# Kernel tuning notes

Hardware: AMD Instinct MI355X
Metric: run time of the kernel (lower is better)

The kernel has to match this reference:

```python
import jax, jax.numpy as jnp
import numpy as np

DIM = 512
NUM_HEADS = 8
HEAD_DIM = DIM // NUM_HEADS
SCALE = HEAD_DIM ** -0.5


def setup_inputs() -> dict:
    key = jax.random.key(0)
    k1, k2, k3, k4 = jax.random.split(key, 4)
    x = jax.random.normal(k1, (2, 4096, DIM), dtype=jnp.float32)
    # Linear weights stored as (in, out) for x @ W; torch Linear(dim, 3*dim, bias=False)
    w_qkv = jax.random.normal(k2, (DIM, 3 * DIM), dtype=jnp.float32) * (DIM ** -0.5)
    w_proj = jax.random.normal(k3, (DIM, DIM), dtype=jnp.float32) * (DIM ** -0.5)
    b_proj = jax.random.normal(k4, (DIM,), dtype=jnp.float32) * 0.02
    return {"x": x, "w_qkv": w_qkv, "w_proj": w_proj, "b_proj": b_proj}


def reference(x, w_qkv, w_proj, b_proj):
    B, N, C = x.shape
    qkv = (x @ w_qkv).reshape(B, N, 3, NUM_HEADS, HEAD_DIM)
    qkv = jnp.transpose(qkv, (2, 0, 3, 1, 4))  # (3, B, H, N, hd)
    q, k, v = qkv[0], qkv[1], qkv[2]
    attn = jnp.einsum("bhnd,bhmd->bhnm", q, k) * SCALE
    attn = jax.nn.softmax(attn, axis=-1)
    out = jnp.einsum("bhnm,bhmd->bhnd", attn, v)
    out = jnp.transpose(out, (0, 2, 1, 3)).reshape(B, N, C)
    return out @ w_proj + b_proj
```

## Files before the change

kernel.cpp:

```cpp
#include <hip/hip_runtime.h>
#include <hip/hip_bf16.h>
#include <stdint.h>
#include <math.h>

#define NC3 1536
#define NC2 1024
#define QSCALE 0.18033688011111907f
#define KSPLIT 2

typedef __attribute__((ext_vector_type(8))) short short8;
typedef __attribute__((ext_vector_type(4))) short short4v;
typedef __attribute__((ext_vector_type(4))) float f32x4;
typedef __attribute__((ext_vector_type(16))) float f32x16;
typedef __attribute__((ext_vector_type(8))) _Float16 f16x8;
typedef __attribute__((ext_vector_type(2))) _Float16 half2v;
typedef __attribute__((ext_vector_type(2))) __fp16 fp16x2;

static __device__ __forceinline__ short f2bf(float f) {
    union { __hip_bfloat16 h; short s; } u;
    u.h = __float2bfloat16(f);
    return u.s;
}
static __device__ __forceinline__ short f2h(float f) {
    union { __fp16 h; short s; } u;
    u.h = (__fp16)f;
    return u.s;
}
static __device__ __forceinline__ unsigned hpack(float a, float b) {
    union { fp16x2 h; unsigned u; } c;
    c.h = __builtin_amdgcn_cvt_pkrtz(a, b);
    return c.u;
}
static __device__ __forceinline__ float dot2acc(unsigned pu, float c) {
    union { unsigned u; half2v h; } a;
    a.u = pu;
#if __has_builtin(__builtin_amdgcn_fdot2)
    half2v one2 = {(_Float16)1.0f, (_Float16)1.0f};
    return __builtin_amdgcn_fdot2(a.h, one2, c, false);
#else
    return c + (float)a.h[0] + (float)a.h[1];
#endif
}

#define GLD_LDS(g, l)                                                          \
    __builtin_amdgcn_global_load_lds(                                          \
        (const __attribute__((address_space(1))) void*)(g),                    \
        (__attribute__((address_space(3))) void*)(l), 16, 0, 0)

__global__ __launch_bounds__(256) void prep(const float* __restrict__ x,
                                            short* __restrict__ xbf,
                                            const float* __restrict__ wqkv,
                                            short* __restrict__ wqkvT,
                                            const float* __restrict__ wproj,
                                            short* __restrict__ wprojT) {
    int tx = threadIdx.x, ty = threadIdx.y;
    int tid = ty * 32 + tx;
    if (blockIdx.z == 0) {
        int bid = blockIdx.y * 48 + blockIdx.x;
        for (int i = bid * 256 + tid; i < 1048576; i += 768 * 256) {
            float4 v = ((const float4*)x)[i];
            short4v o = {f2bf(v.x), f2bf(v.y), f2bf(v.z), f2bf(v.w)};
            ((short4v*)xbf)[i] = o;
        }
        return;
    }
    const float* src;
    short* dst;
    int C;
    bool tof16;
    if (blockIdx.z == 1) { src = wqkv; dst = wqkvT; C = 1536; tof16 = false; }
    else                 { if (blockIdx.x >= 16) return; src = wproj; dst = wprojT; C = 512; tof16 = true; }
    __shared__ short t[32][33];
    int c0 = blockIdx.x * 32, r0 = blockIdx.y * 32;
#pragma unroll
    for (int i = 0; i < 4; i++) {
        float v = src[(size_t)(r0 + ty + i * 8) * C + c0 + tx];
        t[ty + i * 8][tx] = tof16 ? f2h(v) : f2bf(v);
    }
    __syncthreads();
#pragma unroll
    for (int i = 0; i < 4; i++)
        dst[(size_t)(c0 + ty + i * 8) * 512 + r0 + tx] = t[tx][ty + i * 8];
}

__global__ __launch_bounds__(256) void gemm_qkv(const short* __restrict__ A,
                                                const short* __restrict__ Bt,
                                                short* __restrict__ Out,
                                                short* __restrict__ VT) {
    __shared__ __attribute__((aligned(16))) short smem[2][128 * 64];
    short* a_sm = &smem[0][0];
    short* b_sm = &smem[1][0];
    const int tid = threadIdx.x;
    const int lane = tid & 63;
    const int wave = tid >> 6;
    const int wr = wave >> 1, wc = wave & 1;
    const int quad = lane >> 4;
    const int l15 = lane & 15;
    const int orig = blockIdx.y * 64 + blockIdx.x;
    const int xcd = orig & 7;
    const int lid = orig >> 3;
    const int m0 = (xcd * 8 + (lid & 7)) * 128;
    const int n0 = (lid >> 3) * 128;
    const int srow = lane >> 3;
    const int schunk = (lane & 7) ^ srow;

    f32x4 zero4 = {0.f, 0.f, 0.f, 0.f};
    f32x4 acc[4][4];
#pragma unroll
    for (int i = 0; i < 4; i++)
#pragma unroll
        for (int j = 0; j < 4; j++) acc[i][j] = zero4;

    for (int k0 = 0; k0 < 512; k0 += 64) {
        __syncthreads();
#pragma unroll
        for (int i = 0; i < 4; i++) {
            int r0 = wave * 32 + i * 8;
            GLD_LDS(A + (size_t)(m0 + r0 + srow) * 512 + k0 + schunk * 8, a_sm + r0 * 64);
            GLD_LDS(Bt + (size_t)(n0 + r0 + srow) * 512 + k0 + schunk * 8, b_sm + r0 * 64);
        }
        __syncthreads();
#pragma unroll
        for (int kk = 0; kk < 2; kk++) {
            short8 af[4], bfr[4];
#pragma unroll
            for (int mi = 0; mi < 4; mi++) {
                int row = wr * 64 + mi * 16 + l15;
                af[mi] = *(const short8*)(a_sm + row * 64 + (((kk * 4 + quad) ^ (row & 7))) * 8);
            }
#pragma unroll
            for (int ni = 0; ni < 4; ni++) {
                int row = wc * 64 + ni * 16 + l15;
                bfr[ni] = *(const short8*)(b_sm + row * 64 + (((kk * 4 + quad) ^ (row & 7))) * 8);
            }
#pragma unroll
            for (int mi = 0; mi < 4; mi++)
#pragma unroll
                for (int ni = 0; ni < 4; ni++)
                    acc[mi][ni] = __builtin_amdgcn_mfma_f32_16x16x32_bf16(
                        af[mi], bfr[ni], acc[mi][ni], 0, 0, 0);
        }
    }

    if (n0 < 1024) {
#pragma unroll
        for (int mi = 0; mi < 4; mi++) {
#pragma unroll
            for (int ni = 0; ni < 4; ni++) {
                int gm0 = m0 + wr * 64 + mi * 16 + quad * 4;
                int gn = n0 + wc * 64 + ni * 16 + l15;
                f32x4 v = acc[mi][ni];
#pragma unroll
                for (int r = 0; r < 4; r++) {
                    float val = v[r];
                    float o = (gn < 512) ? val * QSCALE : val;
                    Out[(size_t)(gm0 + r) * NC2 + gn] = f2bf(o);
                }
            }
        }
    }

    if (n0 >= 1024) {
        __syncthreads();
        short* lt = &smem[0][0];
        const int sq = ((quad & 1) << 1) | (quad >> 1);
#pragma unroll
        for (int mi = 0; mi < 4; mi++) {
#pragma unroll
            for (int ni = 0; ni < 4; ni++) {
                int cl = wc * 64 + ni * 16 + l15;
                int tg = wr * 16 + mi * 4 + sq;
                int tg2 = tg ^ ((cl & 7) << 1);
                f32x4 v = acc[mi][ni];
                uint2 pk;
                pk.x = hpack(v[0], v[1]);
                pk.y = hpack(v[2], v[3]);
                *(uint2*)(lt + cl * 128 + tg2 * 4) = pk;
            }
        }
        __syncthreads();
        int cl = tid >> 1, half = tid & 1;
        int cv = n0 - 1024 + cl;
        int h = cv >> 6, d = cv & 63;
        int btok = m0 >> 12;
        int mt = m0 & 4095;
        short* vrow = VT + ((size_t)((btok * 8 + h) * 64 + d)) * 4096 + mt + half * 64;
        int m = (cl & 7) << 1;
#pragma unroll
        for (int j = 0; j < 8; j++) {
            int tg = half * 16 + j * 2;
            short8 v8 = *(const short8*)(lt + cl * 128 + (tg ^ m) * 4);
            *(short8*)(vrow + j * 8) = v8;
        }
    }
}

__global__ __launch_bounds__(256, 4) void attn_kernel(const short* __restrict__ QKV,
                                                      const short* __restrict__ VT,
                                                      short* __restrict__ Op0,
                                                      short* __restrict__ Op1,
                                                      float* __restrict__ lpart) {
    __shared__ __attribute__((aligned(16))) short k_sm[2][64 * 64];
    __shared__ __attribute__((aligned(16))) short v_sm[2][64 * 64];

    const int tid = threadIdx.x;
    const int lane = tid & 63;
    const int wave = tid >> 6;
    const int l31 = lane & 31;
    const int hi = lane >> 5;
    const int orig = (blockIdx.z * 16 + blockIdx.y) * 32 + blockIdx.x;
    const int xcd = orig & 7;
    const int lid = orig >> 3;
    const int qt = lid & 31;
    const int pr = xcd * 4 + (lid >> 5);
    const int bh = pr & 15;
    const int ks = pr >> 4;
    const int b = bh >> 3, h = bh & 7;
    const size_t tokbase = (size_t)b * 4096;
    const int rowbase = qt * 128;
    constexpr int NT = 64 / KSPLIT;
    const int kt0 = ks * NT;
    const int kt1 = kt0 + NT;
    const short* Qg = QKV + h * 64;
    const short* Kg = QKV + 512 + h * 64;
    const short* VTg = VT + (size_t)bh * 64 * 4096;
    const int srow = lane >> 3;
    const int schunk = (lane & 7) ^ srow;

    short* qstage = &k_sm[0][0];
#pragma unroll
    for (int i = 0; i < 4; i++) {
        int r0 = wave * 32 + i * 8;
        GLD_LDS(Qg + (tokbase + rowbase + r0 + srow) * NC2 + schunk * 8, qstage + r0 * 64);
    }
    __syncthreads();
    const int qrow = wave * 32 + l31;
    short8 qf[4];
#pragma unroll
    for (int kk = 0; kk < 4; kk++) {
        int slot = (kk * 2 + hi) ^ (qrow & 7);
        qf[kk] = *(const short8*)(qstage + qrow * 64 + slot * 8);
    }
    __syncthreads();

#pragma unroll
    for (int i = 0; i < 2; i++) {
        int r0 = wave * 16 + i * 8;
        GLD_LDS(Kg + (tokbase + (size_t)kt0 * 64 + r0 + srow) * NC2 + schunk * 8,
                k_sm[0] + r0 * 64);
        GLD_LDS(VTg + (size_t)(r0 + srow) * 4096 + kt0 * 64 + schunk * 8,
                v_sm[0] + r0 * 64);
    }

    float zf = 0.f;
    asm volatile("" : "+v"(zf));
    f32x16 zro;
#pragma unroll
    for (int t = 0; t < 16; t++) zro[t] = zf;

    f32x16 acc_o0, acc_o1;
#pragma unroll
    for (int i = 0; i < 16; i++) { acc_o0[i] = 0.f; acc_o1[i] = 0.f; }
    float la0 = 0.f, la1 = 0.f;

    for (int kt = kt0; kt < kt1; kt++) {
        __syncthreads();
        const int cur = kt & 1;
        if (kt < kt1 - 1) {
            const int nb = cur ^ 1;
#pragma unroll
            for (int i = 0; i < 2; i++) {
                int r0 = wave * 16 + i * 8;
                GLD_LDS(Kg + (tokbase + (size_t)(kt + 1) * 64 + r0 + srow) * NC2 + schunk * 8,
                        k_sm[nb] + r0 * 64);
                GLD_LDS(VTg + (size_t)(r0 + srow) * 4096 + (kt + 1) * 64 + schunk * 8,
                        v_sm[nb] + r0 * 64);
            }
        }
        __builtin_amdgcn_s_setprio(1);

        f32x16 s0, s1;
        {
            int slot = hi ^ (l31 & 7);
            short8 kf0 = *(const short8*)(k_sm[cur] + l31 * 64 + slot * 8);
            s0 = __builtin_amdgcn_mfma_f32_32x32x16_bf16(kf0, qf[0], zro, 0, 0, 0);
            short8 kf1 = *(const short8*)(k_sm[cur] + (32 + l31) * 64 + slot * 8);
            s1 = __builtin_amdgcn_mfma_f32_32x32x16_bf16(kf1, qf[0], zro, 0, 0, 0);
        }
#pragma unroll
        for (int kk = 1; kk < 4; kk++) {
            int slot = (kk * 2 + hi) ^ (l31 & 7);
            short8 kf0 = *(const short8*)(k_sm[cur] + l31 * 64 + slot * 8);
            s0 = __builtin_amdgcn_mfma_f32_32x32x16_bf16(kf0, qf[kk], s0, 0, 0, 0);
            short8 kf1 = *(const short8*)(k_sm[cur] + (32 + l31) * 64 + slot * 8);
            s1 = __builtin_amdgcn_mfma_f32_32x32x16_bf16(kf1, qf[kk], s1, 0, 0, 0);
        }

        unsigned pk[2][8];
#pragma unroll
        for (int t = 0; t < 16; t += 2) {
            float e0 = __builtin_amdgcn_exp2f(s0[t]);
            float e1 = __builtin_amdgcn_exp2f(s0[t + 1]);
            unsigned p = hpack(e0, e1);
            pk[0][t >> 1] = p;
            la0 = dot2acc(p, la0);
        }
#pragma unroll
        for (int t = 0; t < 16; t += 2) {
            float e0 = __builtin_amdgcn_exp2f(s1[t]);
            float e1 = __builtin_amdgcn_exp2f(s1[t + 1]);
            unsigned p = hpack(e0, e1);
            pk[1][t >> 1] = p;
            la1 = dot2acc(p, la1);
        }

#pragma unroll
        for (int g = 0; g < 4; g++) {
            union { unsigned u[4]; f16x8 v; } pf;
#pragma unroll
            for (int t = 0; t < 4; t++) pf.u[t] = pk[g >> 1][4 * (g & 1) + t];
            {
                int slot = (g * 2 + hi) ^ (l31 & 7);
                f16x8 vf0 = *(const f16x8*)(v_sm[cur] + l31 * 64 + slot * 8);
                acc_o0 = __builtin_amdgcn_mfma_f32_32x32x16_f16(vf0, pf.v, acc_o0, 0, 0, 0);
                f16x8 vf1 = *(const f16x8*)(v_sm[cur] + (32 + l31) * 64 + slot * 8);
                acc_o1 = __builtin_amdgcn_mfma_f32_32x32x16_f16(vf1, pf.v, acc_o1, 0, 0, 0);
            }
        }
        __builtin_amdgcn_s_setprio(0);
    }

    __syncthreads();

    float l_acc = la0 + la1;
    l_acc += __shfl_xor(l_acc, 32);
    size_t growq = tokbase + rowbase + qrow;
    if (hi == 0) lpart[(size_t)ks * 65536 + growq * 8 + h] = l_acc;

    short* osm = &k_sm[0][0] + wave * 2048;
#pragma unroll
    for (int i = 0; i < 16; i += 2) {
        int d0 = (i & 3) + 8 * (i >> 2) + 4 * hi;
        unsigned pkd0 = hpack(acc_o0[i], acc_o0[i + 1]);
        int slot0 = (d0 >> 3) ^ (l31 & 7);
        *(unsigned*)(osm + l31 * 64 + slot0 * 8 + (d0 & 7)) = pkd0;
        int d1 = 32 + d0;
        unsigned pkd1 = hpack(acc_o1[i], acc_o1[i + 1]);
        int slot1 = (d1 >> 3) ^ (l31 & 7);
        *(unsigned*)(osm + l31 * 64 + slot1 * 8 + (d1 & 7)) = pkd1;
    }
    short* Od = (ks == 0) ? Op0 : Op1;
#pragma unroll
    for (int j = 0; j < 4; j++) {
        int r = lane >> 1;
        int c = (lane & 1) * 4 + j;
        int slot = c ^ (r & 7);
        short8 ov = *(const short8*)(osm + r * 64 + slot * 8);
        size_t grow = tokbase + rowbase + wave * 32 + r;
        *(short8*)(Od + grow * 512 + h * 64 + c * 8) = ov;
    }
}

__global__ __launch_bounds__(256) void gemm_proj(const short* __restrict__ Op0,
                                                 const short* __restrict__ Op1,
                                                 const float* __restrict__ lpart,
                                                 const short* __restrict__ Bt,
                                                 float* __restrict__ OutF,
                                                 const float* __restrict__ bias) {
    __shared__ __attribute__((aligned(16))) short a0_sm[128 * 64];
    __shared__ __attribute__((aligned(16))) short a1_sm[128 * 64];
    __shared__ __attribute__((aligned(16))) short b_sm[64 * 64];
    __shared__ float linv_sm[128 * 8];
    const int tid = threadIdx.x;
    const int lane = tid & 63;
    const int wave = tid >> 6;
    const int wr = wave >> 1, wc = wave & 1;
    const int quad = lane >> 4;
    const int l15 = lane & 15;
    const int orig = blockIdx.y * 64 + blockIdx.x;
    const int xcd = orig & 7;
    const int lid = orig >> 3;
    const int m0 = (xcd * 8 + (lid & 7)) * 128;
    const int n0 = (lid >> 3) * 64;
    const int srow = lane >> 3;
    const int schunk = (lane & 7) ^ srow;

    {
        int idx = tid * 4;
        int row = idx >> 3;
        int hh = idx & 7;
        float4 va = *(const float4*)(lpart + (size_t)(m0 + row) * 8 + hh);
        float4 vb = *(const float4*)(lpart + 65536 + (size_t)(m0 + row) * 8 + hh);
        linv_sm[idx + 0] = 1.0f / (va.x + vb.x);
        linv_sm[idx + 1] = 1.0f / (va.y + vb.y);
        linv_sm[idx + 2] = 1.0f / (va.z + vb.z);
        linv_sm[idx + 3] = 1.0f / (va.w + vb.w);
    }

    f32x4 zero4 = {0.f, 0.f, 0.f, 0.f};
    f32x4 acc[4][2];
#pragma unroll
    for (int i = 0; i < 4; i++) { acc[i][0] = zero4; acc[i][1] = zero4; }

    for (int k0 = 0; k0 < 512; k0 += 64) {
        __syncthreads();
#pragma unroll
        for (int i = 0; i < 4; i++) {
            int r0 = wave * 32 + i * 8;
            GLD_LDS(Op0 + (size_t)(m0 + r0 + srow) * 512 + k0 + schunk * 8, a0_sm + r0 * 64);
            GLD_LDS(Op1 + (size_t)(m0 + r0 + srow) * 512 + k0 + schunk * 8, a1_sm + r0 * 64);
        }
#pragma unroll
        for (int i = 0; i < 2; i++) {
            int r0 = wave * 16 + i * 8;
            GLD_LDS(Bt + (size_t)(n0 + r0 + srow) * 512 + k0 + schunk * 8, b_sm + r0 * 64);
        }
        __syncthreads();
        const int h = k0 >> 6;
#pragma unroll
        for (int kk = 0; kk < 2; kk++) {
            f16x8 af[4], bfr[2];
#pragma unroll
            for (int mi = 0; mi < 4; mi++) {
                int row = wr * 64 + mi * 16 + l15;
                int slot = (kk * 4 + quad) ^ (row & 7);
                f16x8 a0v = *(const f16x8*)(a0_sm + row * 64 + slot * 8);
                f16x8 a1v = *(const f16x8*)(a1_sm + row * 64 + slot * 8);
                _Float16 lh = (_Float16)linv_sm[row * 8 + h];
                f16x8 lv = {lh, lh, lh, lh, lh, lh, lh, lh};
                af[mi] = (a0v + a1v) * lv;
            }
#pragma unroll
            for (int ni = 0; ni < 2; ni++) {
                int row = wc * 32 + ni * 16 + l15;
                int slot = (kk * 4 + quad) ^ (row & 7);
                bfr[ni] = *(const f16x8*)(b_sm + row * 64 + slot * 8);
            }
#pragma unroll
            for (int mi = 0; mi < 4; mi++)
#pragma unroll
                for (int ni = 0; ni < 2; ni++)
                    acc[mi][ni] = __builtin_amdgcn_mfma_f32_16x16x32_f16(
                        af[mi], bfr[ni], acc[mi][ni], 0, 0, 0);
        }
    }

#pragma unroll
    for (int mi = 0; mi < 4; mi++) {
#pragma unroll
        for (int ni = 0; ni < 2; ni++) {
            int gm0 = m0 + wr * 64 + mi * 16 + quad * 4;
            int gn = n0 + wc * 32 + ni * 16 + l15;
            f32x4 v = acc[mi][ni];
#pragma unroll
            for (int r = 0; r < 4; r++)
                OutF[(size_t)(gm0 + r) * 512 + gn] = v[r] + bias[gn];
        }
    }
}

extern "C" void kernel_launch(void* const* d_in, const int* in_sizes, int n_in,
                              void* d_out, int out_size, void* d_ws, size_t ws_size,
                              hipStream_t stream) {
    (void)in_sizes; (void)n_in; (void)out_size; (void)ws_size;
    const float* x = (const float*)d_in[0];
    const float* wqkv = (const float*)d_in[1];
    const float* wproj = (const float*)d_in[2];
    const float* bproj = (const float*)d_in[3];
    float* out = (float*)d_out;

    short* ws = (short*)d_ws;
    short* xbf = ws;
    short* wqkvT = xbf + (size_t)4194304;
    short* wprojT = wqkvT + (size_t)1536 * 512;
    short* QKV = wprojT + (size_t)512 * 512;
    short* VTb = QKV + (size_t)8192 * 1024;
    short* Op0 = VTb + (size_t)16 * 64 * 4096;
    short* Op1 = xbf;
    float* lpart = (float*)wqkvT;

    prep<<<dim3(48, 16, 3), dim3(32, 8), 0, stream>>>(x, xbf, wqkv, wqkvT, wproj, wprojT);
    gemm_qkv<<<dim3(64, 12), 256, 0, stream>>>(xbf, wqkvT, QKV, VTb);
    attn_kernel<<<dim3(32, 16, KSPLIT), 256, 0, stream>>>(QKV, VTb, Op0, Op1, lpart);
    gemm_proj<<<dim3(64, 8), 256, 0, stream>>>(Op0, Op1, lpart, wprojT, out, bproj);
}
```

Before: 196.0 us.

## Split each attention key tile across wave pairs with LDS reduction of partial outputs

The attention kernel now handles 64 query rows per block instead of 128 and launches twice as many blocks. Within a block, pairs of waves share the same 32 query rows and each takes half of every 64-key tile. Each wave runs half the QK and PV MFMAs per tile and holds fewer S registers, which should raise occupancy and parallelism. The cost is reloading each K/V tile for half as many queries, which doubles K/V traffic, plus an end-of-kernel LDS exchange and extra barrier to sum the partial outputs and row sums.

```diff
diff --git a/kernel.cpp b/kernel.cpp
--- a/kernel.cpp
+++ b/kernel.cpp
@@ -208,16 +208,18 @@
     const int wave = tid >> 6;
     const int l31 = lane & 31;
     const int hi = lane >> 5;
-    const int orig = (blockIdx.z * 16 + blockIdx.y) * 32 + blockIdx.x;
+    const int grp = wave >> 1;
+    const int kh = wave & 1;
+    const int orig = (blockIdx.z * 16 + blockIdx.y) * 64 + blockIdx.x;
     const int xcd = orig & 7;
     const int lid = orig >> 3;
-    const int qt = lid & 31;
-    const int pr = xcd * 4 + (lid >> 5);
+    const int qt = lid & 63;
+    const int pr = xcd * 4 + (lid >> 6);
     const int bh = pr & 15;
     const int ks = pr >> 4;
     const int b = bh >> 3, h = bh & 7;
     const size_t tokbase = (size_t)b * 4096;
-    const int rowbase = qt * 128;
+    const int rowbase = qt * 64;
     constexpr int NT = 64 / KSPLIT;
     const int kt0 = ks * NT;
     const int kt1 = kt0 + NT;
@@ -229,17 +231,17 @@
 
     short* qstage = &k_sm[0][0];
 #pragma unroll
-    for (int i = 0; i < 4; i++) {
-        int r0 = wave * 32 + i * 8;
+    for (int i = 0; i < 2; i++) {
+        int r0 = wave * 16 + i * 8;
         GLD_LDS(Qg + (tokbase + rowbase + r0 + srow) * NC2 + schunk * 8, qstage + r0 * 64);
     }
     __syncthreads();
-    const int qrow = wave * 32 + l31;
+    const int qrl = grp * 32 + l31;
     short8 qf[4];
 #pragma unroll
     for (int kk = 0; kk < 4; kk++) {
-        int slot = (kk * 2 + hi) ^ (qrow & 7);
-        qf[kk] = *(const short8*)(qstage + qrow * 64 + slot * 8);
+        int slot = (kk * 2 + hi) ^ (qrl & 7);
+        qf[kk] = *(const short8*)(qstage + qrl * 64 + slot * 8);
     }
     __syncthreads();
 
@@ -261,7 +263,7 @@
     f32x16 acc_o0, acc_o1;
 #pragma unroll
     for (int i = 0; i < 16; i++) { acc_o0[i] = 0.f; acc_o1[i] = 0.f; }
-    float la0 = 0.f, la1 = 0.f;
+    float la = 0.f;
 
     for (int kt = kt0; kt < kt1; kt++) {
         __syncthreads();
@@ -279,85 +281,98 @@
         }
         __builtin_amdgcn_s_setprio(1);
 
-        f32x16 s0, s1;
+        f32x16 s;
         {
             int slot = hi ^ (l31 & 7);
-            short8 kf0 = *(const short8*)(k_sm[cur] + l31 * 64 + slot * 8);
-            s0 = __builtin_amdgcn_mfma_f32_32x32x16_bf16(kf0, qf[0], zro, 0, 0, 0);
-            short8 kf1 = *(const short8*)(k_sm[cur] + (32 + l31) * 64 + slot * 8);
-            s1 = __builtin_amdgcn_mfma_f32_32x32x16_bf16(kf1, qf[0], zro, 0, 0, 0);
+            short8 kf = *(const short8*)(k_sm[cur] + (kh * 32 + l31) * 64 + slot * 8);
+            s = __builtin_amdgcn_mfma_f32_32x32x16_bf16(kf, qf[0], zro, 0, 0, 0);
         }
 #pragma unroll
         for (int kk = 1; kk < 4; kk++) {
             int slot = (kk * 2 + hi) ^ (l31 & 7);
-            short8 kf0 = *(const short8*)(k_sm[cur] + l31 * 64 + slot * 8);
-            s0 = __builtin_amdgcn_mfma_f32_32x32x16_bf16(kf0, qf[kk], s0, 0, 0, 0);
-            short8 kf1 = *(const short8*)(k_sm[cur] + (32 + l31) * 64 + slot * 8);
-            s1 = __builtin_amdgcn_mfma_f32_32x32x16_bf16(kf1, qf[kk], s1, 0, 0, 0);
-        }
-
-        unsigned pk[2][8];
-#pragma unroll
-        for (int t = 0; t < 16; t += 2) {
-            float e0 = __builtin_amdgcn_exp2f(s0[t]);
-            float e1 = __builtin_amdgcn_exp2f(s0[t + 1]);
-            unsigned p = hpack(e0, e1);
-            pk[0][t >> 1] = p;
-            la0 = dot2acc(p, la0);
-        }
-#pragma unroll
-        for (int t = 0; t < 16; t += 2) {
-            float e0 = __builtin_amdgcn_exp2f(s1[t]);
-            float e1 = __builtin_amdgcn_exp2f(s1[t + 1]);
-            unsigned p = hpack(e0, e1);
-            pk[1][t >> 1] = p;
-            la1 = dot2acc(p, la1);
-        }
-
-#pragma unroll
-        for (int g = 0; g < 4; g++) {
+            short8 kf = *(const short8*)(k_sm[cur] + (kh * 32 + l31) * 64 + slot * 8);
+            s = __builtin_amdgcn_mfma_f32_32x32x16_bf16(kf, qf[kk], s, 0, 0, 0);
+        }
+
+        unsigned pk0, pk1, pk2, pk3, pk4, pk5, pk6, pk7;
+#define EXPPAIR(DST, T)                                                        \
+        {                                                                      \
+            float e0 = __builtin_amdgcn_exp2f(s[T]);                           \
+            float e1 = __builtin_amdgcn_exp2f(s[T + 1]);                       \
+            DST = hpack(e0, e1);                                               \
+            la = dot2acc(DST, la);                                             \
+        }
+        EXPPAIR(pk0, 0) EXPPAIR(pk1, 2) EXPPAIR(pk2, 4) EXPPAIR(pk3, 6)
+        EXPPAIR(pk4, 8) EXPPAIR(pk5, 10) EXPPAIR(pk6, 12) EXPPAIR(pk7, 14)
+#undef EXPPAIR
+
+#pragma unroll
+        for (int g = 0; g < 2; g++) {
             union { unsigned u[4]; f16x8 v; } pf;
-#pragma unroll
-            for (int t = 0; t < 4; t++) pf.u[t] = pk[g >> 1][4 * (g & 1) + t];
-            {
-                int slot = (g * 2 + hi) ^ (l31 & 7);
-                f16x8 vf0 = *(const f16x8*)(v_sm[cur] + l31 * 64 + slot * 8);
-                acc_o0 = __builtin_amdgcn_mfma_f32_32x32x16_f16(vf0, pf.v, acc_o0, 0, 0, 0);
-                f16x8 vf1 = *(const f16x8*)(v_sm[cur] + (32 + l31) * 64 + slot * 8);
-                acc_o1 = __builtin_amdgcn_mfma_f32_32x32x16_f16(vf1, pf.v, acc_o1, 0, 0, 0);
-            }
+            if (g == 0) { pf.u[0] = pk0; pf.u[1] = pk1; pf.u[2] = pk2; pf.u[3] = pk3; }
+            else        { pf.u[0] = pk4; pf.u[1] = pk5; pf.u[2] = pk6; pf.u[3] = pk7; }
+            int slot = ((kh * 2 + g) * 2 + hi) ^ (l31 & 7);
+            f16x8 vf0 = *(const f16x8*)(v_sm[cur] + l31 * 64 + slot * 8);
+            acc_o0 = __builtin_amdgcn_mfma_f32_32x32x16_f16(vf0, pf.v, acc_o0, 0, 0, 0);
+            f16x8 vf1 = *(const f16x8*)(v_sm[cur] + (32 + l31) * 64 + slot * 8);
+            acc_o1 = __builtin_amdgcn_mfma_f32_32x32x16_f16(vf1, pf.v, acc_o1, 0, 0, 0);
         }
         __builtin_amdgcn_s_setprio(0);
     }
 
     __syncthreads();
 
-    float l_acc = la0 + la1;
-    l_acc += __shfl_xor(l_acc, 32);
-    size_t growq = tokbase + rowbase + qrow;
-    if (hi == 0) lpart[(size_t)ks * 65536 + growq * 8 + h] = l_acc;
-
-    short* osm = &k_sm[0][0] + wave * 2048;
-#pragma unroll
-    for (int i = 0; i < 16; i += 2) {
-        int d0 = (i & 3) + 8 * (i >> 2) + 4 * hi;
-        unsigned pkd0 = hpack(acc_o0[i], acc_o0[i + 1]);
-        int slot0 = (d0 >> 3) ^ (l31 & 7);
-        *(unsigned*)(osm + l31 * 64 + slot0 * 8 + (d0 & 7)) = pkd0;
-        int d1 = 32 + d0;
-        unsigned pkd1 = hpack(acc_o1[i], acc_o1[i + 1]);
-        int slot1 = (d1 >> 3) ^ (l31 & 7);
-        *(unsigned*)(osm + l31 * 64 + slot1 * 8 + (d1 & 7)) = pkd1;
-    }
-    short* Od = (ks == 0) ? Op0 : Op1;
-#pragma unroll
-    for (int j = 0; j < 4; j++) {
-        int r = lane >> 1;
-        int c = (lane & 1) * 4 + j;
-        int slot = c ^ (r & 7);
-        short8 ov = *(const short8*)(osm + r * 64 + slot * 8);
-        size_t grow = tokbase + rowbase + wave * 32 + r;
-        *(short8*)(Od + grow * 512 + h * 64 + c * 8) = ov;
+    float* xch = (float*)&k_sm[0][0];
+    float* lx = (float*)&v_sm[1][0];
+    if (kh) {
+#pragma unroll
+        for (int c = 0; c < 4; c++) {
+            f32x4 w0 = {acc_o0[c * 4], acc_o0[c * 4 + 1], acc_o0[c * 4 + 2], acc_o0[c * 4 + 3]};
+            *(f32x4*)(xch + (grp * 8 + c) * 256 + lane * 4) = w0;
+            f32x4 w1 = {acc_o1[c * 4], acc_o1[c * 4 + 1], acc_o1[c * 4 + 2], acc_o1[c * 4 + 3]};
+            *(f32x4*)(xch + (grp * 8 + 4 + c) * 256 + lane * 4) = w1;
+        }
+        lx[grp * 64 + lane] = la;
+    }
+    __syncthreads();
+    if (!kh) {
+#pragma unroll
+        for (int c = 0; c < 4; c++) {
+            f32x4 w0 = *(const f32x4*)(xch + (grp * 8 + c) * 256 + lane * 4);
+            acc_o0[c * 4] += w0[0]; acc_o0[c * 4 + 1] += w0[1];
+            acc_o0[c * 4 + 2] += w0[2]; acc_o0[c * 4 + 3] += w0[3];
+            f32x4 w1 = *(const f32x4*)(xch + (grp * 8 + 4 + c) * 256 + lane * 4);
+            acc_o1[c * 4] += w1[0]; acc_o1[c * 4 + 1] += w1[1];
+            acc_o1[c * 4 + 2] += w1[2]; acc_o1[c * 4 + 3] += w1[3];
+        }
+        la += lx[grp * 64 + lane];
+
+        float l_acc = la + __shfl_xor(la, 32);
+        size_t growq = tokbase + rowbase + grp * 32 + l31;
+        if (hi == 0) lpart[(size_t)ks * 65536 + growq * 8 + h] = l_acc;
+
+        short* osm = &v_sm[0][0] + grp * 2048;
+#pragma unroll
+        for (int i = 0; i < 16; i += 2) {
+            int d0 = (i & 3) + 8 * (i >> 2) + 4 * hi;
+            unsigned pkd0 = hpack(acc_o0[i], acc_o0[i + 1]);
+            int slot0 = (d0 >> 3) ^ (l31 & 7);
+            *(unsigned*)(osm + l31 * 64 + slot0 * 8 + (d0 & 7)) = pkd0;
+            int d1 = 32 + d0;
+            unsigned pkd1 = hpack(acc_o1[i], acc_o1[i + 1]);
+            int slot1 = (d1 >> 3) ^ (l31 & 7);
+            *(unsigned*)(osm + l31 * 64 + slot1 * 8 + (d1 & 7)) = pkd1;
+        }
+        short* Od = (ks == 0) ? Op0 : Op1;
+#pragma unroll
+        for (int j = 0; j < 4; j++) {
+            int r = lane >> 1;
+            int c = (lane & 1) * 4 + j;
+            int slot = c ^ (r & 7);
+            short8 ov = *(const short8*)(osm + r * 64 + slot * 8);
+            size_t grow = tokbase + rowbase + grp * 32 + r;
+            *(short8*)(Od + grow * 512 + h * 64 + c * 8) = ov;
+        }
     }
 }
 
@@ -481,6 +496,6 @@
 
     prep<<<dim3(48, 16, 3), dim3(32, 8), 0, stream>>>(x, xbf, wqkv, wqkvT, wproj, wprojT);
     gemm_qkv<<<dim3(64, 12), 256, 0, stream>>>(xbf, wqkvT, QKV, VTb);
-    attn_kernel<<<dim3(32, 16, KSPLIT), 256, 0, stream>>>(QKV, VTb, Op0, Op1, lpart);
+    attn_kernel<<<dim3(64, 16, KSPLIT), 256, 0, stream>>>(QKV, VTb, Op0, Op1, lpart);
     gemm_proj<<<dim3(64, 8), 256, 0, stream>>>(Op0, Op1, lpart, wprojT, out, bproj);
 }
```

New measurement: 201.3 us. 2.7% more time.

## Double K tile to 128 rows and read V directly from global memory

Applied to the files above, without the earlier changes.

The attention loop now stages 128-row K tiles in shared memory, halving the number of iterations and barriers. V tiles are no longer staged in LDS; each wave loads its V^T fragments straight from global memory, relying on L1/L2 caching. This removes the V LDS traffic and the barrier cost per tile. In exchange, the MFMAs now wait directly on global-load latency, and the same V data is reloaded by every wave.

```diff
diff --git a/kernel.cpp b/kernel.cpp
--- a/kernel.cpp
+++ b/kernel.cpp
@@ -200,8 +200,7 @@
                                                       short* __restrict__ Op0,
                                                       short* __restrict__ Op1,
                                                       float* __restrict__ lpart) {
-    __shared__ __attribute__((aligned(16))) short k_sm[2][64 * 64];
-    __shared__ __attribute__((aligned(16))) short v_sm[2][64 * 64];
+    __shared__ __attribute__((aligned(16))) short k_sm[2][128 * 64];
 
     const int tid = threadIdx.x;
     const int lane = tid & 63;
@@ -218,9 +217,9 @@
     const int b = bh >> 3, h = bh & 7;
     const size_t tokbase = (size_t)b * 4096;
     const int rowbase = qt * 128;
-    constexpr int NT = 64 / KSPLIT;
-    const int kt0 = ks * NT;
-    const int kt1 = kt0 + NT;
+    constexpr int NT2 = 32 / KSPLIT;
+    const int kt0 = ks * NT2;
+    const int kt1 = kt0 + NT2;
     const short* Qg = QKV + h * 64;
     const short* Kg = QKV + 512 + h * 64;
     const short* VTg = VT + (size_t)bh * 64 * 4096;
@@ -244,12 +243,10 @@
     __syncthreads();
 
 #pragma unroll
-    for (int i = 0; i < 2; i++) {
-        int r0 = wave * 16 + i * 8;
-        GLD_LDS(Kg + (tokbase + (size_t)kt0 * 64 + r0 + srow) * NC2 + schunk * 8,
+    for (int i = 0; i < 4; i++) {
+        int r0 = wave * 32 + i * 8;
+        GLD_LDS(Kg + (tokbase + (size_t)kt0 * 128 + r0 + srow) * NC2 + schunk * 8,
                 k_sm[0] + r0 * 64);
-        GLD_LDS(VTg + (size_t)(r0 + srow) * 4096 + kt0 * 64 + schunk * 8,
-                v_sm[0] + r0 * 64);
     }
 
     float zf = 0.f;
@@ -263,67 +260,60 @@
     for (int i = 0; i < 16; i++) { acc_o0[i] = 0.f; acc_o1[i] = 0.f; }
     float la0 = 0.f, la1 = 0.f;
 
-    for (int kt = kt0; kt < kt1; kt++) {
-        __syncthreads();
-        const int cur = kt & 1;
-        if (kt < kt1 - 1) {
+#pragma unroll 1
+    for (int t2 = kt0; t2 < kt1; t2++) {
+        __syncthreads();
+        const int cur = (t2 - kt0) & 1;
+        if (t2 < kt1 - 1) {
             const int nb = cur ^ 1;
 #pragma unroll
-            for (int i = 0; i < 2; i++) {
-                int r0 = wave * 16 + i * 8;
-                GLD_LDS(Kg + (tokbase + (size_t)(kt + 1) * 64 + r0 + srow) * NC2 + schunk * 8,
+            for (int i = 0; i < 4; i++) {
+                int r0 = wave * 32 + i * 8;
+                GLD_LDS(Kg + (tokbase + (size_t)(t2 + 1) * 128 + r0 + srow) * NC2 + schunk * 8,
                         k_sm[nb] + r0 * 64);
-                GLD_LDS(VTg + (size_t)(r0 + srow) * 4096 + (kt + 1) * 64 + schunk * 8,
-                        v_sm[nb] + r0 * 64);
             }
         }
         __builtin_amdgcn_s_setprio(1);
-
-        f32x16 s0, s1;
-        {
-            int slot = hi ^ (l31 & 7);
-            short8 kf0 = *(const short8*)(k_sm[cur] + l31 * 64 + slot * 8);
-            s0 = __builtin_amdgcn_mfma_f32_32x32x16_bf16(kf0, qf[0], zro, 0, 0, 0);
-            short8 kf1 = *(const short8*)(k_sm[cur] + (32 + l31) * 64 + slot * 8);
-            s1 = __builtin_amdgcn_mfma_f32_32x32x16_bf16(kf1, qf[0], zro, 0, 0, 0);
-        }
-#pragma unroll
-        for (int kk = 1; kk < 4; kk++) {
-            int slot = (kk * 2 + hi) ^ (l31 & 7);
-            short8 kf0 = *(const short8*)(k_sm[cur] + l31 * 64 + slot * 8);
-            s0 = __builtin_amdgcn_mfma_f32_32x32x16_bf16(kf0, qf[kk], s0, 0, 0, 0);
-            short8 kf1 = *(const short8*)(k_sm[cur] + (32 + l31) * 64 + slot * 8);
-            s1 = __builtin_amdgcn_mfma_f32_32x32x16_bf16(kf1, qf[kk], s1, 0, 0, 0);
-        }
-
-        unsigned pk[2][8];
-#pragma unroll
-        for (int t = 0; t < 16; t += 2) {
-            float e0 = __builtin_amdgcn_exp2f(s0[t]);
-            float e1 = __builtin_amdgcn_exp2f(s0[t + 1]);
-            unsigned p = hpack(e0, e1);
-            pk[0][t >> 1] = p;
-            la0 = dot2acc(p, la0);
-        }
-#pragma unroll
-        for (int t = 0; t < 16; t += 2) {
-            float e0 = __builtin_amdgcn_exp2f(s1[t]);
-            float e1 = __builtin_amdgcn_exp2f(s1[t + 1]);
-            unsigned p = hpack(e0, e1);
-            pk[1][t >> 1] = p;
-            la1 = dot2acc(p, la1);
-        }
-
-#pragma unroll
-        for (int g = 0; g < 4; g++) {
-            union { unsigned u[4]; f16x8 v; } pf;
-#pragma unroll
-            for (int t = 0; t < 4; t++) pf.u[t] = pk[g >> 1][4 * (g & 1) + t];
+        const size_t vtok = (size_t)t2 * 128;
+
+#pragma unroll
+        for (int kb = 0; kb < 4; kb++) {
+            f32x16 s;
             {
-                int slot = (g * 2 + hi) ^ (l31 & 7);
-                f16x8 vf0 = *(const f16x8*)(v_sm[cur] + l31 * 64 + slot * 8);
+                int slot = hi ^ (l31 & 7);
+                short8 kf = *(const short8*)(k_sm[cur] + (kb * 32 + l31) * 64 + slot * 8);
+                s = __builtin_amdgcn_mfma_f32_32x32x16_bf16(kf, qf[0], zro, 0, 0, 0);
+            }
+#pragma unroll
+            for (int kk = 1; kk < 4; kk++) {
+                int slot = (kk * 2 + hi) ^ (l31 & 7);
+                short8 kf = *(const short8*)(k_sm[cur] + (kb * 32 + l31) * 64 + slot * 8);
+                s = __builtin_amdgcn_mfma_f32_32x32x16_bf16(kf, qf[kk], s, 0, 0, 0);
+            }
+
+            unsigned p0, p1, p2, p3, p4, p5, p6, p7;
+            float lkb = 0.f;
+#define EXPPAIR(DST, T)                                                        \
+            {                                                                  \
+                float e0 = __builtin_amdgcn_exp2f(s[T]);                       \
+                float e1 = __builtin_amdgcn_exp2f(s[T + 1]);                   \
+                DST = hpack(e0, e1);                                           \
+                lkb = dot2acc(DST, lkb);                                       \
+            }
+            EXPPAIR(p0, 0) EXPPAIR(p1, 2) EXPPAIR(p2, 4) EXPPAIR(p3, 6)
+            EXPPAIR(p4, 8) EXPPAIR(p5, 10) EXPPAIR(p6, 12) EXPPAIR(p7, 14)
+#undef EXPPAIR
+            if (kb & 1) la1 += lkb; else la0 += lkb;
+
+#pragma unroll
+            for (int gl = 0; gl < 2; gl++) {
+                union { unsigned u[4]; f16x8 v; } pf;
+                if (gl == 0) { pf.u[0] = p0; pf.u[1] = p1; pf.u[2] = p2; pf.u[3] = p3; }
+                else         { pf.u[0] = p4; pf.u[1] = p5; pf.u[2] = p6; pf.u[3] = p7; }
+                int c = kb * 4 + gl * 2 + hi;
+                f16x8 vf0 = *(const f16x8*)(VTg + (size_t)l31 * 4096 + vtok + c * 8);
                 acc_o0 = __builtin_amdgcn_mfma_f32_32x32x16_f16(vf0, pf.v, acc_o0, 0, 0, 0);
-                f16x8 vf1 = *(const f16x8*)(v_sm[cur] + (32 + l31) * 64 + slot * 8);
+                f16x8 vf1 = *(const f16x8*)(VTg + (size_t)(32 + l31) * 4096 + vtok + c * 8);
                 acc_o1 = __builtin_amdgcn_mfma_f32_32x32x16_f16(vf1, pf.v, acc_o1, 0, 0, 0);
             }
         }
```

After: 244.0 us. 24.5% more time.
